# Optimization experiments

Hardware: AMD Instinct MI355X
Metric: run time of the kernel (lower is better)

Reference implementation:

```python
import jax, jax.numpy as jnp
import numpy as np

# Sizes (see init_kwargs / shape_source)
N = 65536      # total points
B = 8          # batch elements
PPB = N // B   # points per batch element (8192, divisible by WS -> no padding)
D = 256        # d_model
H = 8          # nhead
DH = D // H
L = 4          # num_layers
FF = 2048      # torch TransformerEncoderLayer default dim_feedforward
RES = 128      # resolution (coordinate range / embedding table size)
BITS = 7       # ceil(log2(RES)); higher bits of morton loop are zero
WS = 128       # window_size
EPS = 1e-5     # LayerNorm eps


def setup_inputs() -> dict:
    key = jax.random.key(0)
    ks = jax.random.split(key, 16)
    s = 0.02
    batch_col = (jnp.arange(N) // PPB).astype(jnp.int32)
    xyz = jax.random.randint(ks[0], (N, 3), 0, RES, dtype=jnp.int32)
    coords = jnp.concatenate([batch_col[:, None], xyz], axis=1)
    features = jax.random.normal(ks[1], (N, D), jnp.float32)
    inp = {
        'coords': coords,
        'features': features,
        # learned positional embedding tables
        'pe_x': jax.random.normal(ks[2], (RES, D), jnp.float32) * s,
        'pe_y': jax.random.normal(ks[3], (RES, D), jnp.float32) * s,
        'pe_z': jax.random.normal(ks[4], (RES, D), jnp.float32) * s,
        'pe_s': jax.random.normal(ks[5], (RES, D), jnp.float32) * s,
        # stacked transformer encoder layer params (torch post-norm layer)
        'Wqkv': jax.random.normal(ks[6], (L, 3 * D, D), jnp.float32) * s,
        'bqkv': jnp.zeros((L, 3 * D), jnp.float32),
        'Wo': jax.random.normal(ks[7], (L, D, D), jnp.float32) * s,
        'bo': jnp.zeros((L, D), jnp.float32),
        'W1': jax.random.normal(ks[8], (L, FF, D), jnp.float32) * s,
        'b1': jnp.zeros((L, FF), jnp.float32),
        'W2': jax.random.normal(ks[9], (L, D, FF), jnp.float32) * s,
        'b2': jnp.zeros((L, D), jnp.float32),
        'g1': jnp.ones((L, D), jnp.float32),
        'be1': jnp.zeros((L, D), jnp.float32),
        'g2': jnp.ones((L, D), jnp.float32),
        'be2': jnp.zeros((L, D), jnp.float32),
    }
    return inp


def _morton_key(coords):
    # interleave bits of x,y,z (z lowest), prefix with batch index so batch order is preserved
    x, y, z = coords[:, 1], coords[:, 2], coords[:, 3]
    m = jnp.zeros_like(x)
    for i in range(BITS):
        m = m | (((x >> i) & 1) << (3 * i + 2)) \
              | (((y >> i) & 1) << (3 * i + 1)) \
              | (((z >> i) & 1) << (3 * i))
    return coords[:, 0] * (1 << (3 * BITS)) + m


def _ln(x, g, b):
    mu = jnp.mean(x, axis=-1, keepdims=True)
    var = jnp.mean(jnp.square(x - mu), axis=-1, keepdims=True)
    return (x - mu) * jax.lax.rsqrt(var + EPS) * g + b


def _encoder(x, params):
    # x: [Wn, WS, D]; torch TransformerEncoderLayer, post-norm, relu, no dropout (eval)
    scale = float(DH) ** -0.5

    def layer(h, p):
        Wqkv, bqkv, Wo, bo, W1, b1, W2, b2, g1, be1, g2, be2 = p
        Wn = h.shape[0]
        qkv = h @ Wqkv.T + bqkv                      # [Wn, WS, 3D]
        q, k, v = jnp.split(qkv, 3, axis=-1)
        q = q.reshape(Wn, WS, H, DH)
        k = k.reshape(Wn, WS, H, DH)
        v = v.reshape(Wn, WS, H, DH)
        att = jax.nn.softmax(jnp.einsum('wqhd,wkhd->whqk', q, k) * scale, axis=-1)
        o = jnp.einsum('whqk,wkhd->wqhd', att, v).reshape(Wn, WS, D) @ Wo.T + bo
        h = _ln(h + o, g1, be1)
        ff = jax.nn.relu(h @ W1.T + b1) @ W2.T + b2
        h = _ln(h + ff, g2, be2)
        return h, None

    x, _ = jax.lax.scan(layer, x, params)
    return x


def reference(coords, features, pe_x, pe_y, pe_z, pe_s,
              Wqkv, bqkv, Wo, bo, W1, b1, W2, b2, g1, be1, g2, be2):
    # 1) Morton sort (stable, batch-major)
    idx = jnp.argsort(_morton_key(coords))
    sc = coords[idx]
    sf = features[idx]
    # 2) learned positional encoding (stride = 1)
    pe = pe_x[sc[:, 1]] + pe_y[sc[:, 2]] + pe_z[sc[:, 3]] + pe_s[1]
    x = sf + pe
    # 3) window split: PPB % WS == 0, interval == 1 -> exact tiling, no padding
    x = x.reshape(-1, WS, D)                          # [Wn, WS, D]
    # 4) transformer encoder over windows
    x = _encoder(x, (Wqkv, bqkv, Wo, bo, W1, b1, W2, b2, g1, be1, g2, be2))
    # 5) gather back (all masks True -> simple reshape); output in sorted order
    return x.reshape(N, D)
```

## Files before the change

kernel.cpp:

```cpp
#include <hip/hip_runtime.h>

typedef unsigned int u32;
typedef unsigned short u16;

#define NPTS 65536
#define DMODEL 256
#define NHEAD 8
#define DHEAD 32
#define NLAYER 4
#define FFDIM 2048
#define WSIZE 128
#define LNEPS 1e-5f
#define RG 256

#define KSTR 36
#define VSTR 132
#define PSTR 132

typedef __attribute__((ext_vector_type(8))) short short8;
typedef __attribute__((ext_vector_type(4))) float floatx4;

__device__ __forceinline__ float bf2f(u16 v) {
    u32 u = ((u32)v) << 16;
    float f;
    __builtin_memcpy(&f, &u, 4);
    return f;
}
__device__ __forceinline__ u16 f2bf(float f) {
    u32 u;
    __builtin_memcpy(&u, &f, 4);
    u32 r = (u + 0x7fffu + ((u >> 16) & 1u)) >> 16;
    return (u16)r;
}

__device__ __forceinline__ void gl_lds16(const void* g, void* l) {
    __builtin_amdgcn_global_load_lds((const __attribute__((address_space(1))) u32*)g,
                                     (__attribute__((address_space(3))) u32*)l, 16, 0, 0);
}

__global__ __launch_bounds__(256) void morton_kernel(const int* __restrict__ coords,
                                                     u32* __restrict__ key, u32* __restrict__ val) {
    int i = blockIdx.x * 256 + threadIdx.x;
    int b = coords[4 * i + 0];
    int x = coords[4 * i + 1];
    int y = coords[4 * i + 2];
    int z = coords[4 * i + 3];
    u32 m = 0;
#pragma unroll
    for (int t = 0; t < 7; ++t) {
        m |= ((u32)((x >> t) & 1) << (3 * t + 2)) | ((u32)((y >> t) & 1) << (3 * t + 1)) |
             ((u32)((z >> t) & 1) << (3 * t));
    }
    key[i] = ((u32)b << 21) | m;
    val[i] = (u32)i;
}

__global__ __launch_bounds__(256) void hist_kernel(const u32* __restrict__ key, u32* __restrict__ ghist,
                                                   int shift) {
    __shared__ u32 h[256];
    int tid = threadIdx.x;
    h[tid] = 0;
    __syncthreads();
    u32 k = key[blockIdx.x * 256 + tid];
    atomicAdd(&h[(k >> shift) & 255u], 1u);
    __syncthreads();
    ghist[(size_t)tid * RG + blockIdx.x] = h[tid];
}

__global__ __launch_bounds__(256) void scan_up(u32* __restrict__ g, u32* __restrict__ aux) {
    __shared__ u32 wsum[4];
    int tid = threadIdx.x;
    int lane = tid & 63;
    int wave = tid >> 6;
    size_t base = (size_t)blockIdx.x * 1024 + (size_t)tid * 4;
    uint4 v = *(const uint4*)(g + base);
    u32 s = v.x + v.y + v.z + v.w;
    u32 inc = s;
#pragma unroll
    for (int off = 1; off < 64; off <<= 1) {
        u32 u = __shfl_up(inc, off, 64);
        if (lane >= off) inc += u;
    }
    if (lane == 63) wsum[wave] = inc;
    __syncthreads();
    u32 woff = 0;
    for (int w = 0; w < wave; ++w) woff += wsum[w];
    u32 excl = woff + inc - s;
    uint4 o;
    o.x = excl;
    o.y = excl + v.x;
    o.z = excl + v.x + v.y;
    o.w = excl + v.x + v.y + v.z;
    *(uint4*)(g + base) = o;
    if (tid == 255) aux[blockIdx.x] = woff + inc;
}

__global__ __launch_bounds__(256) void scan_down(u32* __restrict__ g, const u32* __restrict__ aux) {
    __shared__ u32 boff;
    int tid = threadIdx.x;
    if (tid < 64) {
        u32 a = (tid < (int)blockIdx.x) ? aux[tid] : 0u;
#pragma unroll
        for (int off = 32; off > 0; off >>= 1) a += __shfl_xor(a, off, 64);
        if (tid == 0) boff = a;
    }
    __syncthreads();
    u32 s = boff;
    size_t base = (size_t)blockIdx.x * 1024 + (size_t)tid * 4;
    uint4 v = *(uint4*)(g + base);
    v.x += s;
    v.y += s;
    v.z += s;
    v.w += s;
    *(uint4*)(g + base) = v;
}

__global__ __launch_bounds__(256) void scatter_kernel(const u32* __restrict__ keyin, const u32* __restrict__ valin,
                                                      u32* __restrict__ keyout, u32* __restrict__ valout,
                                                      const u32* __restrict__ ghist, int shift) {
    __shared__ u32 whist[4][256];
    int tid = threadIdx.x;
    int lane = tid & 63;
    int wave = tid >> 6;
    uint4 z = {0u, 0u, 0u, 0u};
    ((uint4*)&whist[0][0])[tid] = z;
    int gi = blockIdx.x * 256 + tid;
    u32 k = keyin[gi];
    u32 v = valin[gi];
    u32 b = (k >> shift) & 255u;
    __syncthreads();
    unsigned long long m = ~0ull;
#pragma unroll
    for (int bit = 0; bit < 8; ++bit) {
        unsigned long long bb = __ballot((int)((b >> bit) & 1u));
        m &= ((b >> bit) & 1u) ? bb : ~bb;
    }
    unsigned long long below = (lane == 0) ? 0ull : (m & ((1ull << lane) - 1ull));
    int rlane = __popcll(below);
    int cnt = __popcll(m);
    if (rlane == 0) whist[wave][b] = (u32)cnt;
    __syncthreads();
    u32 rank = (u32)rlane;
    for (int w = 0; w < wave; ++w) rank += whist[w][b];
    u32 dst = ghist[(size_t)b * RG + blockIdx.x] + rank;
    keyout[dst] = k;
    valout[dst] = v;
}

__global__ __launch_bounds__(256) void cvt_bf16_kernel(const float* __restrict__ in, u16* __restrict__ out, int n) {
    int i = blockIdx.x * 256 + threadIdx.x;
    if (i < n) out[i] = f2bf(in[i]);
}

template <bool HF32>
__global__ __launch_bounds__(256) void gather_pe_kernel(const u32* __restrict__ idx, const int* __restrict__ coords,
                                                        const float* __restrict__ feat,
                                                        const float* __restrict__ pex, const float* __restrict__ pey,
                                                        const float* __restrict__ pez, const float* __restrict__ pes,
                                                        float* __restrict__ h, u16* __restrict__ xb) {
    int row = blockIdx.x * 4 + (threadIdx.x >> 6);
    int lane = threadIdx.x & 63;
    int src = (int)idx[row];
    int cx = coords[4 * src + 1];
    int cy = coords[4 * src + 2];
    int cz = coords[4 * src + 3];
    int c = lane * 4;
    float4 f = *(const float4*)(feat + (size_t)src * DMODEL + c);
    float4 px = *(const float4*)(pex + (size_t)cx * DMODEL + c);
    float4 py = *(const float4*)(pey + (size_t)cy * DMODEL + c);
    float4 pz = *(const float4*)(pez + (size_t)cz * DMODEL + c);
    float4 ps = *(const float4*)(pes + (size_t)1 * DMODEL + c);
    float4 r;
    r.x = f.x + px.x + py.x + pz.x + ps.x;
    r.y = f.y + px.y + py.y + pz.y + ps.y;
    r.z = f.z + px.z + py.z + pz.z + ps.z;
    r.w = f.w + px.w + py.w + pz.w + ps.w;
    if (HF32) *(float4*)(h + (size_t)row * DMODEL + c) = r;
    ushort4 o;
    o.x = f2bf(r.x);
    o.y = f2bf(r.y);
    o.z = f2bf(r.z);
    o.w = f2bf(r.w);
    *(ushort4*)(xb + (size_t)row * DMODEL + c) = o;
}

__device__ __forceinline__ void stage_tiles(const u16* __restrict__ Abase, const u16* __restrict__ Wbase,
                                            int K, int k0, u16* la, u16* lb, int tid) {
#pragma unroll
    for (int it = 0; it < 4; ++it) {
        int cidx = tid + it * 256;
        int r = cidx >> 3;
        int cc = (cidx & 7) << 3;
        gl_lds16(Abase + (size_t)r * K + k0 + cc, la + cidx * 8);
        gl_lds16(Wbase + (size_t)r * K + k0 + cc, lb + cidx * 8);
    }
}

template <bool RELU, bool BF16OUT>
__global__ __launch_bounds__(256) void gemm_bt(const u16* __restrict__ A, const u16* __restrict__ W,
                                               const float* __restrict__ bias, void* __restrict__ Cout,
                                               int M, int O, int K) {
    __shared__ __align__(16) u16 lA[2][128 * 64];
    __shared__ __align__(16) u16 lB[2][128 * 64];
    const int tid = threadIdx.x;
    const int lane = tid & 63;
    const int wave = tid >> 6;
    const int wr = wave >> 1;
    const int wc = wave & 1;
    const int quad = lane >> 4;
    const int l16 = lane & 15;
    const size_t row0 = (size_t)blockIdx.x * 128;
    const size_t col0 = (size_t)blockIdx.y * 128;
    floatx4 acc[4][4] = {};
    const u16* Abase = A + row0 * (size_t)K;
    const u16* Wbase = W + col0 * (size_t)K;

    const int nt = K >> 6;
    stage_tiles(Abase, Wbase, K, 0, &lA[0][0], &lB[0][0], tid);
    int buf = 0;
    for (int t = 0; t < nt; ++t) {
        if (t + 1 < nt) {
            stage_tiles(Abase, Wbase, K, (t + 1) << 6, &lA[buf ^ 1][0], &lB[buf ^ 1][0], tid);
            asm volatile("s_waitcnt vmcnt(8)" ::: "memory");
        } else {
            asm volatile("s_waitcnt vmcnt(0)" ::: "memory");
        }
        __builtin_amdgcn_s_barrier();
        const u16* la = &lA[buf][0];
        const u16* lb = &lB[buf][0];
#pragma unroll
        for (int kk = 0; kk < 64; kk += 32) {
            short8 af[4], bf[4];
#pragma unroll
            for (int r = 0; r < 4; ++r)
                af[r] = *(const short8*)&la[(wr * 64 + r * 16 + l16) * 64 + kk + quad * 8];
#pragma unroll
            for (int c = 0; c < 4; ++c)
                bf[c] = *(const short8*)&lb[(wc * 64 + c * 16 + l16) * 64 + kk + quad * 8];
#pragma unroll
            for (int r = 0; r < 4; ++r)
#pragma unroll
                for (int c = 0; c < 4; ++c)
                    acc[r][c] = __builtin_amdgcn_mfma_f32_16x16x32_bf16(af[r], bf[c], acc[r][c], 0, 0, 0);
        }
        if (t + 1 < nt) __builtin_amdgcn_s_barrier();
        buf ^= 1;
    }

#pragma unroll
    for (int r = 0; r < 4; ++r) {
#pragma unroll
        for (int c = 0; c < 4; ++c) {
            size_t col = col0 + wc * 64 + c * 16 + l16;
            float bv = bias[col];
#pragma unroll
            for (int reg = 0; reg < 4; ++reg) {
                size_t row = row0 + wr * 64 + r * 16 + quad * 4 + reg;
                float v = acc[r][c][reg] + bv;
                if (RELU) v = fmaxf(v, 0.f);
                if (BF16OUT)
                    ((u16*)Cout)[row * O + col] = f2bf(v);
                else
                    ((float*)Cout)[row * O + col] = v;
            }
        }
    }
}

__global__ __launch_bounds__(128) void attn_kernel(const u16* __restrict__ qkv, u16* __restrict__ outb) {
    const int wh = blockIdx.x;
    const int w = wh >> 3;
    const int h = wh & 7;
    const int tid = threadIdx.x;
    const int wave = tid >> 6;
    const int lane = tid & 63;
    const int quad = lane >> 4;
    const int l16 = lane & 15;
    __shared__ __align__(16) u16 lK[128 * KSTR];
    __shared__ __align__(16) u16 lVt[32 * VSTR];
    __shared__ __align__(16) u16 lP[128 * PSTR];
    const u16* base = qkv + (size_t)w * WSIZE * (3 * DMODEL);

    {
        const u16* krow = base + (size_t)tid * (3 * DMODEL) + DMODEL + h * DHEAD;
        const u16* vrow = base + (size_t)tid * (3 * DMODEL) + 2 * DMODEL + h * DHEAD;
#pragma unroll
        for (int p = 0; p < 4; ++p)
            *(short8*)&lK[tid * KSTR + p * 8] = *(const short8*)(krow + p * 8);
        u16 varr[32];
#pragma unroll
        for (int p = 0; p < 4; ++p)
            *(short8*)&varr[p * 8] = *(const short8*)(vrow + p * 8);
#pragma unroll
        for (int d = 0; d < DHEAD; ++d) lVt[d * VSTR + tid] = varr[d];
    }
    short8 af[4];
#pragma unroll
    for (int mi = 0; mi < 4; ++mi)
        af[mi] = *(const short8*)(base + (size_t)(wave * 64 + mi * 16 + l16) * (3 * DMODEL) + h * DHEAD + quad * 8);
    __syncthreads();

    floatx4 acc[4][8] = {};
#pragma unroll
    for (int ni = 0; ni < 8; ++ni) {
        short8 bk = *(const short8*)&lK[(ni * 16 + l16) * KSTR + quad * 8];
#pragma unroll
        for (int mi = 0; mi < 4; ++mi)
            acc[mi][ni] = __builtin_amdgcn_mfma_f32_16x16x32_bf16(af[mi], bk, acc[mi][ni], 0, 0, 0);
    }

    const float scale = 0.17677669529663687f;
    float inv[4][4];
#pragma unroll
    for (int mi = 0; mi < 4; ++mi) {
#pragma unroll
        for (int reg = 0; reg < 4; ++reg) {
            float m = acc[mi][0][reg];
#pragma unroll
            for (int ni = 1; ni < 8; ++ni) m = fmaxf(m, acc[mi][ni][reg]);
            m = fmaxf(m, __shfl_xor(m, 1, 64));
            m = fmaxf(m, __shfl_xor(m, 2, 64));
            m = fmaxf(m, __shfl_xor(m, 4, 64));
            m = fmaxf(m, __shfl_xor(m, 8, 64));
            float e[8];
            float sum = 0.f;
#pragma unroll
            for (int ni = 0; ni < 8; ++ni) {
                e[ni] = __expf((acc[mi][ni][reg] - m) * scale);
                sum += e[ni];
            }
            sum += __shfl_xor(sum, 1, 64);
            sum += __shfl_xor(sum, 2, 64);
            sum += __shfl_xor(sum, 4, 64);
            sum += __shfl_xor(sum, 8, 64);
            inv[mi][reg] = 1.f / sum;
            int row = wave * 64 + mi * 16 + quad * 4 + reg;
#pragma unroll
            for (int ni = 0; ni < 8; ++ni) lP[row * PSTR + ni * 16 + l16] = f2bf(e[ni]);
        }
    }

    floatx4 acc2[4][2] = {};
#pragma unroll
    for (int kt = 0; kt < 4; ++kt) {
        short8 pa[4];
#pragma unroll
        for (int mi = 0; mi < 4; ++mi)
            pa[mi] = *(const short8*)&lP[(wave * 64 + mi * 16 + l16) * PSTR + kt * 32 + quad * 8];
#pragma unroll
        for (int c = 0; c < 2; ++c) {
            short8 bv = *(const short8*)&lVt[(c * 16 + l16) * VSTR + kt * 32 + quad * 8];
#pragma unroll
            for (int mi = 0; mi < 4; ++mi)
                acc2[mi][c] = __builtin_amdgcn_mfma_f32_16x16x32_bf16(pa[mi], bv, acc2[mi][c], 0, 0, 0);
        }
    }

#pragma unroll
    for (int mi = 0; mi < 4; ++mi) {
#pragma unroll
        for (int c = 0; c < 2; ++c) {
#pragma unroll
            for (int reg = 0; reg < 4; ++reg) {
                int row = wave * 64 + mi * 16 + quad * 4 + reg;
                outb[(size_t)(w * WSIZE + row) * DMODEL + h * DHEAD + c * 16 + l16] =
                    f2bf(acc2[mi][c][reg] * inv[mi][reg]);
            }
        }
    }
}

template <bool HF32, bool OUTF32>
__global__ __launch_bounds__(256) void resid_ln_kernel(const void* __restrict__ hin, const float* __restrict__ delta,
                                                       const float* __restrict__ g, const float* __restrict__ b,
                                                       float* __restrict__ hout, void* __restrict__ nout) {
    int row = blockIdx.x * 4 + (threadIdx.x >> 6);
    int lane = threadIdx.x & 63;
    int c = lane * 4;
    float4 x;
    if (HF32) {
        x = *(const float4*)((const float*)hin + (size_t)row * DMODEL + c);
    } else {
        ushort4 hv = *(const ushort4*)((const u16*)hin + (size_t)row * DMODEL + c);
        x.x = bf2f(hv.x);
        x.y = bf2f(hv.y);
        x.z = bf2f(hv.z);
        x.w = bf2f(hv.w);
    }
    float4 d = *(const float4*)(delta + (size_t)row * DMODEL + c);
    x.x += d.x;
    x.y += d.y;
    x.z += d.z;
    x.w += d.w;
    float s = x.x + x.y + x.z + x.w;
#pragma unroll
    for (int off = 32; off > 0; off >>= 1) s += __shfl_xor(s, off, 64);
    float mu = s * (1.f / 256.f);
    float d0 = x.x - mu, d1 = x.y - mu, d2 = x.z - mu, d3 = x.w - mu;
    float vs = d0 * d0 + d1 * d1 + d2 * d2 + d3 * d3;
#pragma unroll
    for (int off = 32; off > 0; off >>= 1) vs += __shfl_xor(vs, off, 64);
    float rs = rsqrtf(vs * (1.f / 256.f) + LNEPS);
    float4 gg = *(const float4*)(g + c);
    float4 bb = *(const float4*)(b + c);
    float4 y;
    y.x = d0 * rs * gg.x + bb.x;
    y.y = d1 * rs * gg.y + bb.y;
    y.z = d2 * rs * gg.z + bb.z;
    y.w = d3 * rs * gg.w + bb.w;
    if (HF32) *(float4*)(hout + (size_t)row * DMODEL + c) = y;
    if (OUTF32) {
        *(float4*)((float*)nout + (size_t)row * DMODEL + c) = y;
    } else {
        ushort4 o;
        o.x = f2bf(y.x);
        o.y = f2bf(y.y);
        o.z = f2bf(y.z);
        o.w = f2bf(y.w);
        *(ushort4*)((u16*)nout + (size_t)row * DMODEL + c) = o;
    }
}

extern "C" void kernel_launch(void* const* d_in, const int* in_sizes, int n_in,
                              void* d_out, int out_size, void* d_ws, size_t ws_size,
                              hipStream_t stream) {
    (void)in_sizes;
    (void)n_in;
    (void)out_size;
    const int* coords = (const int*)d_in[0];
    const float* feat = (const float*)d_in[1];
    const float* pex = (const float*)d_in[2];
    const float* pey = (const float*)d_in[3];
    const float* pez = (const float*)d_in[4];
    const float* pes = (const float*)d_in[5];
    const float* Wqkv = (const float*)d_in[6];
    const float* bqkv = (const float*)d_in[7];
    const float* Wo = (const float*)d_in[8];
    const float* bo = (const float*)d_in[9];
    const float* W1 = (const float*)d_in[10];
    const float* b1 = (const float*)d_in[11];
    const float* W2 = (const float*)d_in[12];
    const float* b2 = (const float*)d_in[13];
    const float* g1 = (const float*)d_in[14];
    const float* be1 = (const float*)d_in[15];
    const float* g2 = (const float*)d_in[16];
    const float* be2 = (const float*)d_in[17];

    auto al = [](size_t x) { return (x + 255) & ~(size_t)255; };
    const size_t sortB = 4 * al((size_t)NPTS * 4) + al((size_t)256 * RG * 4) + 256;
    const size_t wqkvB = al((size_t)NLAYER * 3 * DMODEL * DMODEL * 2);
    const size_t woB = al((size_t)NLAYER * DMODEL * DMODEL * 2);
    const size_t w1B = al((size_t)NLAYER * FFDIM * DMODEL * 2);
    const size_t w2B = al((size_t)NLAYER * DMODEL * FFDIM * 2);
    const size_t wB = wqkvB + woB + w1B + w2B;
    const size_t xbB = al((size_t)NPTS * DMODEL * 2);
    const size_t hB = al((size_t)NPTS * DMODEL * 4);

    int CH = 0;
    bool modeA = true;
    for (int ch = 65536; ch >= 128; ch >>= 1) {
        size_t need = sortB + wB + xbB + hB + al((size_t)ch * 4096) + al((size_t)ch * 1024) + 65536;
        if (need <= ws_size) { CH = ch; modeA = true; break; }
    }
    if (!CH) {
        for (int ch = 65536; ch >= 128; ch >>= 1) {
            size_t need = sortB + wB + xbB + al((size_t)ch * 4096) + al((size_t)ch * 1024) + 65536;
            if (need <= ws_size) { CH = ch; modeA = false; break; }
        }
    }
    if (!CH) { CH = 128; modeA = false; }

    char* ws = (char*)d_ws;
    size_t off = 0;
    auto alloc = [&](size_t bytes) -> void* {
        void* p = ws + off;
        off += al(bytes);
        return p;
    };
    u32* key0 = (u32*)alloc(NPTS * 4);
    u32* val0 = (u32*)alloc(NPTS * 4);
    u32* key1 = (u32*)alloc(NPTS * 4);
    u32* val1 = (u32*)alloc(NPTS * 4);
    u32* ghist = (u32*)alloc(256 * RG * 4);
    u32* aux = (u32*)alloc(64 * 4);
    u16* wqkv_b = (u16*)alloc((size_t)NLAYER * 3 * DMODEL * DMODEL * 2);
    u16* wo_b = (u16*)alloc((size_t)NLAYER * DMODEL * DMODEL * 2);
    u16* w1_b = (u16*)alloc((size_t)NLAYER * FFDIM * DMODEL * 2);
    u16* w2_b = (u16*)alloc((size_t)NLAYER * DMODEL * FFDIM * 2);
    u16* xb = (u16*)alloc((size_t)NPTS * DMODEL * 2);
    float* h = modeA ? (float*)alloc((size_t)NPTS * DMODEL * 4) : nullptr;
    u16* scratch1 = (u16*)alloc((size_t)CH * 4096);
    float* tmpc = (float*)alloc((size_t)CH * 1024);

    morton_kernel<<<NPTS / 256, 256, 0, stream>>>(coords, key0, val0);

    u32 *ki = key0, *vi = val0, *ko = key1, *vo = val1;
    for (int p = 0; p < 3; ++p) {
        hist_kernel<<<RG, 256, 0, stream>>>(ki, ghist, p * 8);
        scan_up<<<64, 256, 0, stream>>>(ghist, aux);
        scan_down<<<64, 256, 0, stream>>>(ghist, aux);
        scatter_kernel<<<RG, 256, 0, stream>>>(ki, vi, ko, vo, ghist, p * 8);
        u32* t;
        t = ki; ki = ko; ko = t;
        t = vi; vi = vo; vo = t;
    }
    const u32* idx = vi;

    cvt_bf16_kernel<<<(NLAYER * 3 * DMODEL * DMODEL) / 256, 256, 0, stream>>>(Wqkv, wqkv_b, NLAYER * 3 * DMODEL * DMODEL);
    cvt_bf16_kernel<<<(NLAYER * DMODEL * DMODEL) / 256, 256, 0, stream>>>(Wo, wo_b, NLAYER * DMODEL * DMODEL);
    cvt_bf16_kernel<<<(NLAYER * FFDIM * DMODEL) / 256, 256, 0, stream>>>(W1, w1_b, NLAYER * FFDIM * DMODEL);
    cvt_bf16_kernel<<<(NLAYER * DMODEL * FFDIM) / 256, 256, 0, stream>>>(W2, w2_b, NLAYER * DMODEL * FFDIM);

    if (modeA)
        gather_pe_kernel<true><<<NPTS / 4, 256, 0, stream>>>(idx, coords, feat, pex, pey, pez, pes, h, xb);
    else
        gather_pe_kernel<false><<<NPTS / 4, 256, 0, stream>>>(idx, coords, feat, pex, pey, pez, pes, nullptr, xb);

    const int nch = NPTS / CH;
    u16* qkvc = scratch1;
    u16* attoutc = scratch1 + (size_t)CH * 768;
    u16* midc = scratch1;
    for (int l = 0; l < NLAYER; ++l) {
        for (int c = 0; c < nch; ++c) {
            u16* xc = xb + (size_t)c * CH * DMODEL;
            float* hc = modeA ? h + (size_t)c * CH * DMODEL : nullptr;
            gemm_bt<false, true><<<dim3(CH / 128, (3 * DMODEL) / 128), 256, 0, stream>>>(
                xc, wqkv_b + (size_t)l * 3 * DMODEL * DMODEL, bqkv + (size_t)l * 3 * DMODEL, qkvc,
                CH, 3 * DMODEL, DMODEL);
            attn_kernel<<<(CH / WSIZE) * NHEAD, 128, 0, stream>>>(qkvc, attoutc);
            gemm_bt<false, false><<<dim3(CH / 128, DMODEL / 128), 256, 0, stream>>>(
                attoutc, wo_b + (size_t)l * DMODEL * DMODEL, bo + (size_t)l * DMODEL, tmpc,
                CH, DMODEL, DMODEL);
            if (modeA)
                resid_ln_kernel<true, false><<<CH / 4, 256, 0, stream>>>(hc, tmpc, g1 + (size_t)l * DMODEL,
                                                                         be1 + (size_t)l * DMODEL, hc, xc);
            else
                resid_ln_kernel<false, false><<<CH / 4, 256, 0, stream>>>(xc, tmpc, g1 + (size_t)l * DMODEL,
                                                                          be1 + (size_t)l * DMODEL, nullptr, xc);
            gemm_bt<true, true><<<dim3(CH / 128, FFDIM / 128), 256, 0, stream>>>(
                xc, w1_b + (size_t)l * FFDIM * DMODEL, b1 + (size_t)l * FFDIM, midc,
                CH, FFDIM, DMODEL);
            gemm_bt<false, false><<<dim3(CH / 128, DMODEL / 128), 256, 0, stream>>>(
                midc, w2_b + (size_t)l * DMODEL * FFDIM, b2 + (size_t)l * DMODEL, tmpc,
                CH, DMODEL, FFDIM);
            bool last = (l == NLAYER - 1);
            void* outc = last ? (void*)((float*)d_out + (size_t)c * CH * DMODEL) : (void*)xc;
            if (modeA) {
                if (last)
                    resid_ln_kernel<true, true><<<CH / 4, 256, 0, stream>>>(hc, tmpc, g2 + (size_t)l * DMODEL,
                                                                            be2 + (size_t)l * DMODEL, hc, outc);
                else
                    resid_ln_kernel<true, false><<<CH / 4, 256, 0, stream>>>(hc, tmpc, g2 + (size_t)l * DMODEL,
                                                                             be2 + (size_t)l * DMODEL, hc, outc);
            } else {
                if (last)
                    resid_ln_kernel<false, true><<<CH / 4, 256, 0, stream>>>(xc, tmpc, g2 + (size_t)l * DMODEL,
                                                                             be2 + (size_t)l * DMODEL, nullptr, outc);
                else
                    resid_ln_kernel<false, false><<<CH / 4, 256, 0, stream>>>(xc, tmpc, g2 + (size_t)l * DMODEL,
                                                                              be2 + (size_t)l * DMODEL, nullptr, outc);
            }
        }
    }
}
```

Measured before the change: 2.634 ms.

## Split-K the FFN down-projection, swizzle GEMM block order, fold scan_down into scatter

The W2 GEMM (K=2048) is now split across two z-slices that write separate fp32 partial buffers, and the following residual+LayerNorm kernel sums both partials, so the small-grid GEMM gets more blocks. GEMM blocks along x are remapped with a stride-8 swizzle, likely to spread neighbouring row tiles across XCDs. The radix sort's scan_down launch is removed: scatter computes the block-prefix of aux itself and adds it to the histogram offset. The cost is extra fp32 partial traffic and workspace for split-K, plus one more kernel parameter.

```diff
diff --git a/kernel.cpp b/kernel.cpp
--- a/kernel.cpp
+++ b/kernel.cpp
@@ -95,35 +95,27 @@
     if (tid == 255) aux[blockIdx.x] = woff + inc;
 }
 
-__global__ __launch_bounds__(256) void scan_down(u32* __restrict__ g, const u32* __restrict__ aux) {
-    __shared__ u32 boff;
-    int tid = threadIdx.x;
-    if (tid < 64) {
-        u32 a = (tid < (int)blockIdx.x) ? aux[tid] : 0u;
-#pragma unroll
-        for (int off = 32; off > 0; off >>= 1) a += __shfl_xor(a, off, 64);
-        if (tid == 0) boff = a;
-    }
-    __syncthreads();
-    u32 s = boff;
-    size_t base = (size_t)blockIdx.x * 1024 + (size_t)tid * 4;
-    uint4 v = *(uint4*)(g + base);
-    v.x += s;
-    v.y += s;
-    v.z += s;
-    v.w += s;
-    *(uint4*)(g + base) = v;
-}
-
 __global__ __launch_bounds__(256) void scatter_kernel(const u32* __restrict__ keyin, const u32* __restrict__ valin,
                                                       u32* __restrict__ keyout, u32* __restrict__ valout,
-                                                      const u32* __restrict__ ghist, int shift) {
+                                                      const u32* __restrict__ ghist, const u32* __restrict__ aux,
+                                                      int shift) {
     __shared__ u32 whist[4][256];
+    __shared__ u32 apre[64];
     int tid = threadIdx.x;
     int lane = tid & 63;
     int wave = tid >> 6;
     uint4 z = {0u, 0u, 0u, 0u};
     ((uint4*)&whist[0][0])[tid] = z;
+    if (tid < 64) {
+        u32 a = aux[tid];
+        u32 inc = a;
+#pragma unroll
+        for (int off = 1; off < 64; off <<= 1) {
+            u32 u = __shfl_up(inc, off, 64);
+            if (lane >= off) inc += u;
+        }
+        apre[tid] = inc - a;
+    }
     int gi = blockIdx.x * 256 + tid;
     u32 k = keyin[gi];
     u32 v = valin[gi];
@@ -142,7 +134,8 @@
     __syncthreads();
     u32 rank = (u32)rlane;
     for (int w = 0; w < wave; ++w) rank += whist[w][b];
-    u32 dst = ghist[(size_t)b * RG + blockIdx.x] + rank;
+    u32 e = b * (u32)RG + blockIdx.x;
+    u32 dst = ghist[e] + apre[e >> 10] + rank;
     keyout[dst] = k;
     valout[dst] = v;
 }
@@ -209,13 +202,18 @@
     const int wc = wave & 1;
     const int quad = lane >> 4;
     const int l16 = lane & 15;
-    const size_t row0 = (size_t)blockIdx.x * 128;
+    u32 gx = gridDim.x;
+    u32 bx = blockIdx.x;
+    if ((gx & 7u) == 0u) bx = (bx & 7u) * (gx >> 3) + (bx >> 3);
+    const int kz = blockIdx.z;
+    const int Kpart = K / (int)gridDim.z;
+    const size_t row0 = (size_t)bx * 128;
     const size_t col0 = (size_t)blockIdx.y * 128;
     floatx4 acc[4][4] = {};
-    const u16* Abase = A + row0 * (size_t)K;
-    const u16* Wbase = W + col0 * (size_t)K;
-
-    const int nt = K >> 6;
+    const u16* Abase = A + row0 * (size_t)K + (size_t)kz * Kpart;
+    const u16* Wbase = W + col0 * (size_t)K + (size_t)kz * Kpart;
+
+    const int nt = Kpart >> 6;
     stage_tiles(Abase, Wbase, K, 0, &lA[0][0], &lB[0][0], tid);
     int buf = 0;
     for (int t = 0; t < nt; ++t) {
@@ -247,12 +245,13 @@
         buf ^= 1;
     }
 
+    float* Cf = (float*)Cout + (size_t)kz * ((size_t)M * O);
 #pragma unroll
     for (int r = 0; r < 4; ++r) {
 #pragma unroll
         for (int c = 0; c < 4; ++c) {
             size_t col = col0 + wc * 64 + c * 16 + l16;
-            float bv = bias[col];
+            float bv = (kz == 0) ? bias[col] : 0.f;
 #pragma unroll
             for (int reg = 0; reg < 4; ++reg) {
                 size_t row = row0 + wr * 64 + r * 16 + quad * 4 + reg;
@@ -261,7 +260,7 @@
                 if (BF16OUT)
                     ((u16*)Cout)[row * O + col] = f2bf(v);
                 else
-                    ((float*)Cout)[row * O + col] = v;
+                    Cf[row * O + col] = v;
             }
         }
     }
@@ -370,10 +369,11 @@
     }
 }
 
-template <bool HF32, bool OUTF32>
+template <bool HF32, bool OUTF32, int NS>
 __global__ __launch_bounds__(256) void resid_ln_kernel(const void* __restrict__ hin, const float* __restrict__ delta,
                                                        const float* __restrict__ g, const float* __restrict__ b,
-                                                       float* __restrict__ hout, void* __restrict__ nout) {
+                                                       float* __restrict__ hout, void* __restrict__ nout,
+                                                       size_t dstride) {
     int row = blockIdx.x * 4 + (threadIdx.x >> 6);
     int lane = threadIdx.x & 63;
     int c = lane * 4;
@@ -388,6 +388,13 @@
         x.w = bf2f(hv.w);
     }
     float4 d = *(const float4*)(delta + (size_t)row * DMODEL + c);
+    if (NS == 2) {
+        float4 d2 = *(const float4*)(delta + dstride + (size_t)row * DMODEL + c);
+        d.x += d2.x;
+        d.y += d2.y;
+        d.z += d2.z;
+        d.w += d2.w;
+    }
     x.x += d.x;
     x.y += d.y;
     x.z += d.z;
@@ -456,19 +463,23 @@
     const size_t xbB = al((size_t)NPTS * DMODEL * 2);
     const size_t hB = al((size_t)NPTS * DMODEL * 4);
 
-    int CH = 0;
+    int CH = 0, KSP = 1;
     bool modeA = true;
-    for (int ch = 65536; ch >= 128; ch >>= 1) {
-        size_t need = sortB + wB + xbB + hB + al((size_t)ch * 4096) + al((size_t)ch * 1024) + 65536;
-        if (need <= ws_size) { CH = ch; modeA = true; break; }
+    for (int ch = 65536; ch >= 128 && !CH; ch >>= 1) {
+        for (int ksp = 2; ksp >= 1; --ksp) {
+            size_t need = sortB + wB + xbB + hB + al((size_t)ch * 4096) + al((size_t)ch * 1024 * ksp) + 65536;
+            if (need <= ws_size) { CH = ch; KSP = ksp; modeA = true; break; }
+        }
     }
     if (!CH) {
-        for (int ch = 65536; ch >= 128; ch >>= 1) {
-            size_t need = sortB + wB + xbB + al((size_t)ch * 4096) + al((size_t)ch * 1024) + 65536;
-            if (need <= ws_size) { CH = ch; modeA = false; break; }
-        }
-    }
-    if (!CH) { CH = 128; modeA = false; }
+        for (int ch = 65536; ch >= 128 && !CH; ch >>= 1) {
+            for (int ksp = 2; ksp >= 1; --ksp) {
+                size_t need = sortB + wB + xbB + al((size_t)ch * 4096) + al((size_t)ch * 1024 * ksp) + 65536;
+                if (need <= ws_size) { CH = ch; KSP = ksp; modeA = false; break; }
+            }
+        }
+    }
+    if (!CH) { CH = 128; KSP = 1; modeA = false; }
 
     char* ws = (char*)d_ws;
     size_t off = 0;
@@ -490,7 +501,8 @@
     u16* xb = (u16*)alloc((size_t)NPTS * DMODEL * 2);
     float* h = modeA ? (float*)alloc((size_t)NPTS * DMODEL * 4) : nullptr;
     u16* scratch1 = (u16*)alloc((size_t)CH * 4096);
-    float* tmpc = (float*)alloc((size_t)CH * 1024);
+    float* tmpc = (float*)alloc((size_t)CH * 1024 * KSP);
+    const size_t dstride = (size_t)CH * DMODEL;
 
     morton_kernel<<<NPTS / 256, 256, 0, stream>>>(coords, key0, val0);
 
@@ -498,8 +510,7 @@
     for (int p = 0; p < 3; ++p) {
         hist_kernel<<<RG, 256, 0, stream>>>(ki, ghist, p * 8);
         scan_up<<<64, 256, 0, stream>>>(ghist, aux);
-        scan_down<<<64, 256, 0, stream>>>(ghist, aux);
-        scatter_kernel<<<RG, 256, 0, stream>>>(ki, vi, ko, vo, ghist, p * 8);
+        scatter_kernel<<<RG, 256, 0, stream>>>(ki, vi, ko, vo, ghist, aux, p * 8);
         u32* t;
         t = ki; ki = ko; ko = t;
         t = vi; vi = vo; vo = t;
@@ -532,33 +543,51 @@
                 attoutc, wo_b + (size_t)l * DMODEL * DMODEL, bo + (size_t)l * DMODEL, tmpc,
                 CH, DMODEL, DMODEL);
             if (modeA)
-                resid_ln_kernel<true, false><<<CH / 4, 256, 0, stream>>>(hc, tmpc, g1 + (size_t)l * DMODEL,
-                                                                         be1 + (size_t)l * DMODEL, hc, xc);
+                resid_ln_kernel<true, false, 1><<<CH / 4, 256, 0, stream>>>(hc, tmpc, g1 + (size_t)l * DMODEL,
+                                                                            be1 + (size_t)l * DMODEL, hc, xc, dstride);
             else
-                resid_ln_kernel<false, false><<<CH / 4, 256, 0, stream>>>(xc, tmpc, g1 + (size_t)l * DMODEL,
-                                                                          be1 + (size_t)l * DMODEL, nullptr, xc);
+                resid_ln_kernel<false, false, 1><<<CH / 4, 256, 0, stream>>>(xc, tmpc, g1 + (size_t)l * DMODEL,
+                                                                             be1 + (size_t)l * DMODEL, nullptr, xc, dstride);
             gemm_bt<true, true><<<dim3(CH / 128, FFDIM / 128), 256, 0, stream>>>(
                 xc, w1_b + (size_t)l * FFDIM * DMODEL, b1 + (size_t)l * FFDIM, midc,
                 CH, FFDIM, DMODEL);
-            gemm_bt<false, false><<<dim3(CH / 128, DMODEL / 128), 256, 0, stream>>>(
+            gemm_bt<false, false><<<dim3(CH / 128, DMODEL / 128, KSP), 256, 0, stream>>>(
                 midc, w2_b + (size_t)l * DMODEL * FFDIM, b2 + (size_t)l * DMODEL, tmpc,
                 CH, DMODEL, FFDIM);
             bool last = (l == NLAYER - 1);
             void* outc = last ? (void*)((float*)d_out + (size_t)c * CH * DMODEL) : (void*)xc;
             if (modeA) {
-                if (last)
-                    resid_ln_kernel<true, true><<<CH / 4, 256, 0, stream>>>(hc, tmpc, g2 + (size_t)l * DMODEL,
-                                                                            be2 + (size_t)l * DMODEL, hc, outc);
-                else
-                    resid_ln_kernel<true, false><<<CH / 4, 256, 0, stream>>>(hc, tmpc, g2 + (size_t)l * DMODEL,
-                                                                             be2 + (size_t)l * DMODEL, hc, outc);
+                if (last) {
+                    if (KSP == 2)
+                        resid_ln_kernel<true, true, 2><<<CH / 4, 256, 0, stream>>>(hc, tmpc, g2 + (size_t)l * DMODEL,
+                                                                                   be2 + (size_t)l * DMODEL, hc, outc, dstride);
+                    else
+                        resid_ln_kernel<true, true, 1><<<CH / 4, 256, 0, stream>>>(hc, tmpc, g2 + (size_t)l * DMODEL,
+                                                                                   be2 + (size_t)l * DMODEL, hc, outc, dstride);
+                } else {
+                    if (KSP == 2)
+                        resid_ln_kernel<true, false, 2><<<CH / 4, 256, 0, stream>>>(hc, tmpc, g2 + (size_t)l * DMODEL,
+                                                                                    be2 + (size_t)l * DMODEL, hc, outc, dstride);
+                    else
+                        resid_ln_kernel<true, false, 1><<<CH / 4, 256, 0, stream>>>(hc, tmpc, g2 + (size_t)l * DMODEL,
+                                                                                    be2 + (size_t)l * DMODEL, hc, outc, dstride);
+                }
             } else {
-                if (last)
-                    resid_ln_kernel<false, true><<<CH / 4, 256, 0, stream>>>(xc, tmpc, g2 + (size_t)l * DMODEL,
-                                                                             be2 + (size_t)l * DMODEL, nullptr, outc);
-                else
-                    resid_ln_kernel<false, false><<<CH / 4, 256, 0, stream>>>(xc, tmpc, g2 + (size_t)l * DMODEL,
-                                                                              be2 + (size_t)l * DMODEL, nullptr, outc);
+                if (last) {
+                    if (KSP == 2)
+                        resid_ln_kernel<false, true, 2><<<CH / 4, 256, 0, stream>>>(xc, tmpc, g2 + (size_t)l * DMODEL,
+                                                                                    be2 + (size_t)l * DMODEL, nullptr, outc, dstride);
+                    else
+                        resid_ln_kernel<false, true, 1><<<CH / 4, 256, 0, stream>>>(xc, tmpc, g2 + (size_t)l * DMODEL,
+                                                                                    be2 + (size_t)l * DMODEL, nullptr, outc, dstride);
+                } else {
+                    if (KSP == 2)
+                        resid_ln_kernel<false, false, 2><<<CH / 4, 256, 0, stream>>>(xc, tmpc, g2 + (size_t)l * DMODEL,
+                                                                                     be2 + (size_t)l * DMODEL, nullptr, outc, dstride);
+                    else
+                        resid_ln_kernel<false, false, 1><<<CH / 4, 256, 0, stream>>>(xc, tmpc, g2 + (size_t)l * DMODEL,
+                                                                                     be2 + (size_t)l * DMODEL, nullptr, outc, dstride);
+                }
             }
         }
     }
```

New measurement: 2.698 ms. 2.4% more time.
